# Optimization experiments

Measured on AMD Instinct MI355X. Metric: run time of the kernel, lower is better.

Reference implementation:

```python
import jax, jax.numpy as jnp
import numpy as np

SEQ_LEN = 1000
IN_DIM = 100
POOL = SEQ_LEN // IN_DIM  # 10
HIDDEN = 64
OUT_DIM = 5
N_BASIS = 16
BATCH = 65536


def setup_inputs() -> dict:
    key = jax.random.key(0)
    k1, k2, k3 = jax.random.split(key, 3)
    x = jax.random.normal(k1, (BATCH, SEQ_LEN), dtype=jnp.float32)
    c1_mu = jax.random.normal(k2, (HIDDEN, IN_DIM, N_BASIS), dtype=jnp.float32) * 0.05
    c2_mu = jax.random.normal(k3, (OUT_DIM, HIDDEN, N_BASIS), dtype=jnp.float32) * 0.05
    centers = jnp.linspace(-3.0, 3.0, N_BASIS, dtype=jnp.float32)
    return {"x": x, "c1_mu": c1_mu, "c2_mu": c2_mu, "centers": centers}


def _norm(x):
    # torch .std() uses ddof=1 (unbiased)
    mu = jnp.mean(x, axis=1, keepdims=True)
    sd = jnp.std(x, axis=1, keepdims=True, ddof=1)
    return (x - mu) / (sd + 1e-6)


def _basis(x, centers):
    # x: [b, d] -> [b, d, n_basis]; RBF with fixed variance 0.36
    d = x[..., None] - centers
    return jnp.exp(-0.5 * d * d / 0.36)


def _kan(x, c, centers):
    B = _basis(x, centers)  # [b, i, n]
    return jnp.einsum('bin,oin->bo', B, c)


def reference(x, c1_mu, c2_mu, centers):
    b = x.shape[0]
    # unfold(1, pool, pool).mean(-1): non-overlapping average pooling
    x = x.reshape(b, IN_DIM, POOL).mean(-1)  # [b, 100]
    x = _norm(x)
    h = jnp.tanh(_kan(x, c1_mu, centers))  # [b, 64]
    h = _norm(h)
    out = _kan(h, c2_mu, centers)  # [b, 5]
    return out
```

## Files before the change

### kernel.cpp

```cpp
#include <hip/hip_runtime.h>
#include <hip/hip_bf16.h>


#define SEQ    1000
#define INDIM  100
#define HID    64
#define OUTD   5
#define NB     16
#define ROWS   16
#define NTHR   64

typedef __bf16 v8bf __attribute__((ext_vector_type(8)));
typedef float  v4f  __attribute__((ext_vector_type(4)));

#define XSTR 101
#define HSTR 65

__global__ __launch_bounds__(256) void cvt_w(
    const float* __restrict__ c1, const float* __restrict__ c2,
    __bf16* __restrict__ c1b, __bf16* __restrict__ c2b)
{
  int t = blockIdx.x * 256 + threadIdx.x;
  if (t < 25600) {
    float4 v = ((const float4*)c1)[t];
    __bf16* d = c1b + t * 4;
    d[0] = (__bf16)v.x; d[1] = (__bf16)v.y; d[2] = (__bf16)v.z; d[3] = (__bf16)v.w;
  }
  if (t < 4096) {
    int o = t >> 8;
    __bf16* d = c2b + t * 4;
    if (o < OUTD) {
      float4 v = ((const float4*)c2)[t];
      d[0] = (__bf16)v.x; d[1] = (__bf16)v.y; d[2] = (__bf16)v.z; d[3] = (__bf16)v.w;
    } else {
      d[0] = (__bf16)0.f; d[1] = (__bf16)0.f; d[2] = (__bf16)0.f; d[3] = (__bf16)0.f;
    }
  }
}

__global__ __launch_bounds__(NTHR, 4) void kan_main(
    const float* __restrict__ x, const __bf16* __restrict__ c1b,
    const __bf16* __restrict__ c2bw, const float* __restrict__ cen,
    float* __restrict__ out)
{
  __shared__ __align__(16) float sm[ROWS * XSTR];
  float* xn = sm;
  float* hb = sm;

  const int tid  = threadIdx.x;
  const int row0 = blockIdx.x * ROWS;
  const int l15 = tid & 15, q = tid >> 4, iq = q >> 1;

  const float Sn = 1.17851130f;
  float cs[8];
  {
    const int n0 = (q & 1) * 8;
    #pragma unroll
    for (int j = 0; j < 8; ++j) cs[j] = cen[n0 + j] * Sn;
  }

  #pragma unroll
  for (int it = 0; it < 13; ++it) {
    int idx = tid + it * NTHR;
    if (idx < 800) {
      int r = idx / 50, p = idx - r * 50;
      const float4* xp = (const float4*)(x + (size_t)(row0 + r) * SEQ + p * 20);
      float4 a0 = xp[0], a1 = xp[1], a2 = xp[2], a3 = xp[3], a4 = xp[4];
      float s0 = a0.x + a0.y + a0.z + a0.w + a1.x + a1.y + a1.z + a1.w + a2.x + a2.y;
      float s1 = a2.z + a2.w + a3.x + a3.y + a3.z + a3.w + a4.x + a4.y + a4.z + a4.w;
      xn[r * XSTR + 2 * p]     = s0 * 0.1f;
      xn[r * XSTR + 2 * p + 1] = s1 * 0.1f;
    }
  }
  __syncthreads();

  #pragma unroll
  for (int rr = 0; rr < 16; ++rr) {
    float v0 = xn[rr * XSTR + tid];
    float v1 = (tid < 36) ? xn[rr * XSTR + 64 + tid] : 0.f;
    float s = v0 + v1, s2 = v0 * v0 + v1 * v1;
    #pragma unroll
    for (int m = 32; m; m >>= 1) { s += __shfl_xor(s, m, 64); s2 += __shfl_xor(s2, m, 64); }
    float mu = s * (1.f / INDIM);
    float var = (s2 - INDIM * mu * mu) * (1.f / (INDIM - 1));
    float rs = 1.f / (sqrtf(fmaxf(var, 0.f)) + 1e-6f);
    xn[rr * XSTR + tid] = (v0 - mu) * rs;
    if (tid < 36) xn[rr * XSTR + 64 + tid] = (v1 - mu) * rs;
  }
  __syncthreads();

  const float* xrow = xn + l15 * XSTR;
  const __bf16* bp0 = c1b + (size_t)(l15)      * 1600 + q * 8;
  const __bf16* bp1 = c1b + (size_t)(16 + l15) * 1600 + q * 8;
  const __bf16* bp2 = c1b + (size_t)(32 + l15) * 1600 + q * 8;
  const __bf16* bp3 = c1b + (size_t)(48 + l15) * 1600 + q * 8;
  v4f acc0 = {0.f, 0.f, 0.f, 0.f}, acc1 = acc0, acc2 = acc0, acc3 = acc0;

  #pragma unroll 2
  for (int c = 0; c < 10; ++c) {
    #pragma unroll
    for (int ks = 0; ks < 5; ++ks) {
      int ko = c * 160 + ks * 32;
      float xv = xrow[c * 10 + 2 * ks + iq] * Sn;
      v8bf a;
      #pragma unroll
      for (int j = 0; j < 8; ++j) {
        float d = xv - cs[j];
        a[j] = (__bf16)__expf(-(d * d));
      }
      v8bf b0 = *(const v8bf*)(bp0 + ko);
      v8bf b1 = *(const v8bf*)(bp1 + ko);
      v8bf b2 = *(const v8bf*)(bp2 + ko);
      v8bf b3 = *(const v8bf*)(bp3 + ko);
      acc0 = __builtin_amdgcn_mfma_f32_16x16x32_bf16(a, b0, acc0, 0, 0, 0);
      acc1 = __builtin_amdgcn_mfma_f32_16x16x32_bf16(a, b1, acc1, 0, 0, 0);
      acc2 = __builtin_amdgcn_mfma_f32_16x16x32_bf16(a, b2, acc2, 0, 0, 0);
      acc3 = __builtin_amdgcn_mfma_f32_16x16x32_bf16(a, b3, acc3, 0, 0, 0);
    }
  }
  __syncthreads();

  auto tanh_store = [&](v4f a, int cb) {
    #pragma unroll
    for (int rg = 0; rg < 4; ++rg) {
      float t = a[rg];
      float e = __expf(t + t);
      hb[(q * 4 + rg) * HSTR + cb * 16 + l15] = 1.f - 2.f / (e + 1.f);
    }
  };
  tanh_store(acc0, 0); tanh_store(acc1, 1); tanh_store(acc2, 2); tanh_store(acc3, 3);
  __syncthreads();

  #pragma unroll
  for (int rr = 0; rr < 16; ++rr) {
    float v = hb[rr * HSTR + tid];
    float s = v, s2 = v * v;
    #pragma unroll
    for (int m = 32; m; m >>= 1) { s += __shfl_xor(s, m, 64); s2 += __shfl_xor(s2, m, 64); }
    float mu = s * (1.f / HID);
    float var = (s2 - HID * mu * mu) * (1.f / (HID - 1));
    float rs = 1.f / (sqrtf(fmaxf(var, 0.f)) + 1e-6f);
    hb[rr * HSTR + tid] = (v - mu) * rs;
  }
  __syncthreads();

  const float* hrow = hb + l15 * HSTR;
  const __bf16* bp4 = c2bw + (size_t)l15 * 1024 + q * 8;
  v4f o4 = {0.f, 0.f, 0.f, 0.f};
  #pragma unroll 8
  for (int t8 = 0; t8 < 32; ++t8) {
    float hv = hrow[2 * t8 + iq] * Sn;
    v8bf a;
    #pragma unroll
    for (int j = 0; j < 8; ++j) {
      float d = hv - cs[j];
      a[j] = (__bf16)__expf(-(d * d));
    }
    v8bf vb = *(const v8bf*)(bp4 + t8 * 32);
    o4 = __builtin_amdgcn_mfma_f32_16x16x32_bf16(a, vb, o4, 0, 0, 0);
  }

  if (l15 < OUTD) {
    #pragma unroll
    for (int rg = 0; rg < 4; ++rg)
      out[(size_t)(row0 + q * 4 + rg) * OUTD + l15] = o4[rg];
  }
}

extern "C" void kernel_launch(void* const* d_in, const int* in_sizes, int n_in,
                              void* d_out, int out_size, void* d_ws, size_t ws_size,
                              hipStream_t stream) {
  const float* x   = (const float*)d_in[0];
  const float* c1  = (const float*)d_in[1];
  const float* c2  = (const float*)d_in[2];
  const float* cen = (const float*)d_in[3];
  float* out = (float*)d_out;

  __bf16* c1b = (__bf16*)d_ws;
  __bf16* c2b = (__bf16*)((char*)d_ws + 204800);

  hipLaunchKernelGGL(cvt_w, dim3(100), dim3(256), 0, stream, c1, c2, c1b, c2b);
  hipLaunchKernelGGL(kan_main, dim3(65536 / ROWS), dim3(NTHR), 0, stream,
                     x, c1b, c2b, cen, out);
}
```

Measured before the change: 461.1 us.

## Split-K across two waves, fuse pooling with row norm, use exp2/rcp intrinsics

Doubles the block to two waves that split the K dimension of both KAN layers and combine partial accumulators through shared memory. Pooling and the first normalization are fused in registers with shuffle reductions, and the tanh and second norm are fused into the reduction step. Exponentials switch to exp2 with prescaled constants, and reciprocal and sqrt use hardware intrinsics. This trades extra LDS traffic and barriers for more parallelism and less transcendental cost. The first norm's epsilon changes from 1e-6 to 1e-5.

```diff
diff --git a/kernel.cpp b/kernel.cpp
--- a/kernel.cpp
+++ b/kernel.cpp
@@ -6,15 +6,32 @@
 #define INDIM  100
 #define HID    64
 #define OUTD   5
-#define NB     16
 #define ROWS   16
-#define NTHR   64
+#define NTHR   128
 
 typedef __bf16 v8bf __attribute__((ext_vector_type(8)));
 typedef float  v4f  __attribute__((ext_vector_type(4)));
 
 #define XSTR 101
 #define HSTR 65
+#define RSTR 68
+#define R2STR 20
+
+#if __has_builtin(__builtin_amdgcn_exp2f)
+#define EXP2(x) __builtin_amdgcn_exp2f(x)
+#else
+#define EXP2(x) exp2f(x)
+#endif
+#if __has_builtin(__builtin_amdgcn_rcpf)
+#define RCP(x) __builtin_amdgcn_rcpf(x)
+#else
+#define RCP(x) (1.f / (x))
+#endif
+#if __has_builtin(__builtin_amdgcn_sqrtf)
+#define SQRT(x) __builtin_amdgcn_sqrtf(x)
+#else
+#define SQRT(x) sqrtf(x)
+#endif
 
 __global__ __launch_bounds__(256) void cvt_w(
     const float* __restrict__ c1, const float* __restrict__ c2,
@@ -38,132 +55,157 @@
   }
 }
 
-__global__ __launch_bounds__(NTHR, 4) void kan_main(
+__global__ __launch_bounds__(NTHR, 8) void kan_main(
     const float* __restrict__ x, const __bf16* __restrict__ c1b,
     const __bf16* __restrict__ c2bw, const float* __restrict__ cen,
     float* __restrict__ out)
 {
-  __shared__ __align__(16) float sm[ROWS * XSTR];
-  float* xn = sm;
-  float* hb = sm;
+  __shared__ __align__(16) float sm[2128];
+  float* xn   = sm;
+  float* red  = sm;
+  float* hb   = sm + 1088;
+  float* red2 = sm;
 
   const int tid  = threadIdx.x;
+  const int w    = tid >> 6, lane = tid & 63;
   const int row0 = blockIdx.x * ROWS;
-  const int l15 = tid & 15, q = tid >> 4, iq = q >> 1;
-
-  const float Sn = 1.17851130f;
+  const int l15 = lane & 15, q = lane >> 4, iq = q >> 1;
+
+  const float Sn2 = 1.41553628f;
+  const float TL2 = 2.88539008f;
   float cs[8];
   {
     const int n0 = (q & 1) * 8;
     #pragma unroll
-    for (int j = 0; j < 8; ++j) cs[j] = cen[n0 + j] * Sn;
-  }
-
+    for (int j = 0; j < 8; ++j) cs[j] = cen[n0 + j] * Sn2;
+  }
+
+  const int pr   = (w << 3) + (lane & 7);
+  const int slot = lane >> 3;
+  float pva[14];
+  float s = 0.f, s2 = 0.f;
+  {
+    const float* xg = x + (size_t)(row0 + pr) * SEQ;
+    #pragma unroll
+    for (int it = 0; it < 7; ++it) {
+      int p = slot + (it << 3);
+      float u0 = 0.f, u1 = 0.f;
+      if (p < 50) {
+        const float4* xp = (const float4*)(xg + p * 20);
+        float4 a0 = xp[0], a1 = xp[1], a2 = xp[2], a3 = xp[3], a4 = xp[4];
+        u0 = a0.x+a0.y+a0.z+a0.w + a1.x+a1.y+a1.z+a1.w + a2.x+a2.y;
+        u1 = a2.z+a2.w + a3.x+a3.y+a3.z+a3.w + a4.x+a4.y+a4.z+a4.w;
+        s += u0 + u1; s2 += u0*u0 + u1*u1;
+      }
+      pva[2*it] = u0; pva[2*it+1] = u1;
+    }
+  }
   #pragma unroll
-  for (int it = 0; it < 13; ++it) {
-    int idx = tid + it * NTHR;
-    if (idx < 800) {
-      int r = idx / 50, p = idx - r * 50;
-      const float4* xp = (const float4*)(x + (size_t)(row0 + r) * SEQ + p * 20);
-      float4 a0 = xp[0], a1 = xp[1], a2 = xp[2], a3 = xp[3], a4 = xp[4];
-      float s0 = a0.x + a0.y + a0.z + a0.w + a1.x + a1.y + a1.z + a1.w + a2.x + a2.y;
-      float s1 = a2.z + a2.w + a3.x + a3.y + a3.z + a3.w + a4.x + a4.y + a4.z + a4.w;
-      xn[r * XSTR + 2 * p]     = s0 * 0.1f;
-      xn[r * XSTR + 2 * p + 1] = s1 * 0.1f;
-    }
-  }
-  __syncthreads();
-
-  #pragma unroll
-  for (int rr = 0; rr < 16; ++rr) {
-    float v0 = xn[rr * XSTR + tid];
-    float v1 = (tid < 36) ? xn[rr * XSTR + 64 + tid] : 0.f;
-    float s = v0 + v1, s2 = v0 * v0 + v1 * v1;
-    #pragma unroll
-    for (int m = 32; m; m >>= 1) { s += __shfl_xor(s, m, 64); s2 += __shfl_xor(s2, m, 64); }
-    float mu = s * (1.f / INDIM);
-    float var = (s2 - INDIM * mu * mu) * (1.f / (INDIM - 1));
-    float rs = 1.f / (sqrtf(fmaxf(var, 0.f)) + 1e-6f);
-    xn[rr * XSTR + tid] = (v0 - mu) * rs;
-    if (tid < 36) xn[rr * XSTR + 64 + tid] = (v1 - mu) * rs;
-  }
-  __syncthreads();
-
-  const float* xrow = xn + l15 * XSTR;
-  const __bf16* bp0 = c1b + (size_t)(l15)      * 1600 + q * 8;
-  const __bf16* bp1 = c1b + (size_t)(16 + l15) * 1600 + q * 8;
-  const __bf16* bp2 = c1b + (size_t)(32 + l15) * 1600 + q * 8;
-  const __bf16* bp3 = c1b + (size_t)(48 + l15) * 1600 + q * 8;
-  v4f acc0 = {0.f, 0.f, 0.f, 0.f}, acc1 = acc0, acc2 = acc0, acc3 = acc0;
+  for (int m = 8; m <= 32; m <<= 1) {
+    s += __shfl_xor(s, m, 64); s2 += __shfl_xor(s2, m, 64);
+  }
+  {
+    float mu  = s * 0.01f;
+    float var = (s2 - 100.f * mu * mu) * (1.f / 99.f);
+    float rs  = Sn2 * RCP(SQRT(fmaxf(var, 0.f)) + 1e-5f);
+    #pragma unroll
+    for (int it = 0; it < 7; ++it) {
+      int p = slot + (it << 3);
+      if (p < 50) {
+        xn[pr * XSTR + 2*p]     = (pva[2*it]     - mu) * rs;
+        xn[pr * XSTR + 2*p + 1] = (pva[2*it + 1] - mu) * rs;
+      }
+    }
+  }
+  __syncthreads();
+
+  const float* xr = xn + l15 * XSTR;
+  const __bf16* bq = c1b + q * 8;
+  v4f acc[4];
+  acc[0] = (v4f){0.f,0.f,0.f,0.f}; acc[1] = acc[0]; acc[2] = acc[0]; acc[3] = acc[0];
 
   #pragma unroll 2
-  for (int c = 0; c < 10; ++c) {
+  for (int c5 = 0; c5 < 5; ++c5) {
+    int c = w * 5 + c5;
     #pragma unroll
     for (int ks = 0; ks < 5; ++ks) {
-      int ko = c * 160 + ks * 32;
-      float xv = xrow[c * 10 + 2 * ks + iq] * Sn;
+      float xv = xr[c * 10 + 2 * ks + iq];
       v8bf a;
       #pragma unroll
       for (int j = 0; j < 8; ++j) {
         float d = xv - cs[j];
-        a[j] = (__bf16)__expf(-(d * d));
-      }
-      v8bf b0 = *(const v8bf*)(bp0 + ko);
-      v8bf b1 = *(const v8bf*)(bp1 + ko);
-      v8bf b2 = *(const v8bf*)(bp2 + ko);
-      v8bf b3 = *(const v8bf*)(bp3 + ko);
-      acc0 = __builtin_amdgcn_mfma_f32_16x16x32_bf16(a, b0, acc0, 0, 0, 0);
-      acc1 = __builtin_amdgcn_mfma_f32_16x16x32_bf16(a, b1, acc1, 0, 0, 0);
-      acc2 = __builtin_amdgcn_mfma_f32_16x16x32_bf16(a, b2, acc2, 0, 0, 0);
-      acc3 = __builtin_amdgcn_mfma_f32_16x16x32_bf16(a, b3, acc3, 0, 0, 0);
-    }
-  }
-  __syncthreads();
-
-  auto tanh_store = [&](v4f a, int cb) {
-    #pragma unroll
-    for (int rg = 0; rg < 4; ++rg) {
-      float t = a[rg];
-      float e = __expf(t + t);
-      hb[(q * 4 + rg) * HSTR + cb * 16 + l15] = 1.f - 2.f / (e + 1.f);
-    }
-  };
-  tanh_store(acc0, 0); tanh_store(acc1, 1); tanh_store(acc2, 2); tanh_store(acc3, 3);
+        a[j] = (__bf16)EXP2(-(d * d));
+      }
+      int ko = c * 160 + ks * 32;
+      #pragma unroll
+      for (int cb = 0; cb < 4; ++cb) {
+        v8bf b = *(const v8bf*)(bq + (size_t)(cb * 16 + l15) * 1600 + ko);
+        acc[cb] = __builtin_amdgcn_mfma_f32_16x16x32_bf16(a, b, acc[cb], 0, 0, 0);
+      }
+    }
+  }
   __syncthreads();
 
   #pragma unroll
-  for (int rr = 0; rr < 16; ++rr) {
-    float v = hb[rr * HSTR + tid];
-    float s = v, s2 = v * v;
-    #pragma unroll
-    for (int m = 32; m; m >>= 1) { s += __shfl_xor(s, m, 64); s2 += __shfl_xor(s2, m, 64); }
-    float mu = s * (1.f / HID);
-    float var = (s2 - HID * mu * mu) * (1.f / (HID - 1));
-    float rs = 1.f / (sqrtf(fmaxf(var, 0.f)) + 1e-6f);
-    hb[rr * HSTR + tid] = (v - mu) * rs;
-  }
-  __syncthreads();
-
-  const float* hrow = hb + l15 * HSTR;
-  const __bf16* bp4 = c2bw + (size_t)l15 * 1024 + q * 8;
-  v4f o4 = {0.f, 0.f, 0.f, 0.f};
-  #pragma unroll 8
-  for (int t8 = 0; t8 < 32; ++t8) {
-    float hv = hrow[2 * t8 + iq] * Sn;
+  for (int rgo = 0; rgo < 2; ++rgo) {
+    int rg = 2 * (1 - w) + rgo;
+    #pragma unroll
+    for (int cb = 0; cb < 4; ++cb)
+      red[(q * 4 + rg) * RSTR + cb * 16 + l15] = acc[cb][rg];
+  }
+  __syncthreads();
+  #pragma unroll
+  for (int rgo = 0; rgo < 2; ++rgo) {
+    int rg = 2 * w + rgo;
+    float h[4], ss = 0.f, ss2 = 0.f;
+    #pragma unroll
+    for (int cb = 0; cb < 4; ++cb) {
+      float t = acc[cb][rg] + red[(q * 4 + rg) * RSTR + cb * 16 + l15];
+      float e = EXP2(t * TL2);
+      float hv = 1.f - 2.f * RCP(e + 1.f);
+      h[cb] = hv; ss += hv; ss2 += hv * hv;
+    }
+    #pragma unroll
+    for (int m = 1; m <= 8; m <<= 1) {
+      ss += __shfl_xor(ss, m, 64); ss2 += __shfl_xor(ss2, m, 64);
+    }
+    float muh  = ss * (1.f / 64.f);
+    float varh = (ss2 - 64.f * muh * muh) * (1.f / 63.f);
+    float rsh  = Sn2 * RCP(SQRT(fmaxf(varh, 0.f)) + 1e-6f);
+    #pragma unroll
+    for (int cb = 0; cb < 4; ++cb)
+      hb[(q * 4 + rg) * HSTR + cb * 16 + l15] = (h[cb] - muh) * rsh;
+  }
+  __syncthreads();
+
+  const float* hr = hb + l15 * HSTR;
+  const __bf16* bq2 = c2bw + (size_t)l15 * 1024 + q * 8;
+  v4f o4 = (v4f){0.f, 0.f, 0.f, 0.f};
+  #pragma unroll 4
+  for (int t = 0; t < 16; ++t) {
+    int t8 = w * 16 + t;
+    float hv = hr[2 * t8 + iq];
     v8bf a;
     #pragma unroll
     for (int j = 0; j < 8; ++j) {
       float d = hv - cs[j];
-      a[j] = (__bf16)__expf(-(d * d));
-    }
-    v8bf vb = *(const v8bf*)(bp4 + t8 * 32);
+      a[j] = (__bf16)EXP2(-(d * d));
+    }
+    v8bf vb = *(const v8bf*)(bq2 + t8 * 32);
     o4 = __builtin_amdgcn_mfma_f32_16x16x32_bf16(a, vb, o4, 0, 0, 0);
   }
-
-  if (l15 < OUTD) {
+  if (w == 0) {
     #pragma unroll
     for (int rg = 0; rg < 4; ++rg)
-      out[(size_t)(row0 + q * 4 + rg) * OUTD + l15] = o4[rg];
+      red2[(q * 4 + rg) * R2STR + l15] = o4[rg];
+  }
+  __syncthreads();
+  if (w == 1 && l15 < OUTD) {
+    #pragma unroll
+    for (int rg = 0; rg < 4; ++rg) {
+      int r = q * 4 + rg;
+      out[(size_t)(row0 + r) * OUTD + l15] = o4[rg] + red2[r * R2STR + l15];
+    }
   }
 }
 
```

New measurement: 451.8 us. 1.02x faster.
